# Optimization experiments

Hardware: AMD Instinct MI355X
Metric: run time of the kernel (lower is better)

Reference implementation:

```python
import jax, jax.numpy as jnp
import numpy as np

EPS = 1e-12  # tf.nn.l2_normalize epsilon
ALPHA = 0.9  # hard-negative threshold factor (function default)


def l2_normalize(x):
    # matches tf.nn.l2_normalize: x / sqrt(max(sum(x^2), eps))
    return x * jax.lax.rsqrt(jnp.maximum(jnp.sum(x * x, axis=-1, keepdims=True), EPS))


def setup_inputs() -> dict:
    key = jax.random.key(0)
    k1, k2, k3, k4, k5 = jax.random.split(key, 5)
    B, N, K, D, C = 16, 8, 2048, 512, 11
    return {
        "predicted_vectors": jax.random.normal(k1, (B, C, D), dtype=jnp.float32),
        "positive_vectors": jax.random.normal(k2, (B, N, D), dtype=jnp.float32),
        "negative_gallery": jax.random.normal(k3, (B, N, K, D), dtype=jnp.float32),
        "cluster_centers": jax.random.normal(k4, (C, D), dtype=jnp.float32),
        "positive_categories": jax.random.randint(k5, (B, N), 0, 12, dtype=jnp.int32),
    }


def reference(predicted_vectors, positive_vectors, negative_gallery, cluster_centers, positive_categories):
    # center-base combined contrastive loss (IQON3000, categories 1-11)
    cat_idx = jnp.clip(positive_categories - 1, 0, 10)                 # (B, N)
    # gather predicted slot per category: (B, N, D)
    pred_sel = jnp.take_along_axis(predicted_vectors, cat_idx[..., None], axis=1)
    centers = cluster_centers[cat_idx]                                  # (B, N, D)
    pred_norm = l2_normalize(pred_sel - centers)                        # (B, N, D)
    pos_norm = l2_normalize(positive_vectors - centers)                 # (B, N, D)
    neg_norm = l2_normalize(negative_gallery - centers[:, :, None, :])  # (B, N, K, D)

    sim_pos = jnp.sum(pred_norm * pos_norm, axis=-1)                    # (B, N)
    sim_neg = jnp.einsum('bnd,bnkd->bnk', pred_norm, neg_norm)          # (B, N, K)

    thresh = ALPHA * sim_pos[..., None]
    hard_mask = (sim_neg - sim_pos[..., None] >= thresh).astype(jnp.float32)

    exp_pos = jnp.exp(sim_pos)                                          # sims bounded in [-1,1]
    neg_sum = jnp.sum(jnp.exp(sim_neg) * hard_mask, axis=-1)
    denom = jnp.maximum(exp_pos + neg_sum, 1e-7)
    loss = -jnp.log(exp_pos / denom)
    return jnp.mean(loss)
```

## Files before the change

kernel.cpp:

```cpp
#include <hip/hip_runtime.h>
#include <math.h>

#define BB 16
#define NN 8
#define KK 2048
#define DD 512
#define CC 11
#define BN (BB*NN)
#define NCHUNK 16
#define KCHUNK (KK/NCHUNK)
#define EPSN 1e-12f
#define ALPHA 0.9f

struct f8 { float v[8]; };

__device__ __forceinline__ f8 load8(const float* base, int l) {
    const float4* p = (const float4*)base;
    float4 x = p[l];
    float4 y = p[l + 64];
    f8 r;
    r.v[0] = x.x; r.v[1] = x.y; r.v[2] = x.z; r.v[3] = x.w;
    r.v[4] = y.x; r.v[5] = y.y; r.v[6] = y.z; r.v[7] = y.w;
    return r;
}

__device__ __forceinline__ float wave_reduce(float v) {
    #pragma unroll
    for (int off = 1; off < 64; off <<= 1)
        v += __shfl_xor(v, off, 64);
    return v;
}

__device__ __forceinline__ int clamp_cat(int c) {
    c = c - 1;
    return c < 0 ? 0 : (c > 10 ? 10 : c);
}

__global__ __launch_bounds__(64)
void k1_simpos(const float* __restrict__ pred, const float* __restrict__ pos,
               const float* __restrict__ centers, const int* __restrict__ cats,
               float* __restrict__ simpos) {
    int bn = blockIdx.x;
    int b  = bn / NN;
    int l  = threadIdx.x;
    int cat = clamp_cat(cats[bn]);

    f8 pr = load8(pred + ((size_t)b * CC + cat) * DD, l);
    f8 cc = load8(centers + (size_t)cat * DD, l);
    f8 po = load8(pos + (size_t)bn * DD, l);

    float ssa = 0.f, ssb = 0.f;
    float a[8], p[8];
    #pragma unroll
    for (int j = 0; j < 8; ++j) {
        a[j] = pr.v[j] - cc.v[j];
        p[j] = po.v[j] - cc.v[j];
        ssa += a[j] * a[j];
        ssb += p[j] * p[j];
    }
    ssa = wave_reduce(ssa);
    ssb = wave_reduce(ssb);
    float ia = 1.0f / sqrtf(fmaxf(ssa, EPSN));
    float ib = 1.0f / sqrtf(fmaxf(ssb, EPSN));

    float dp = 0.f;
    #pragma unroll
    for (int j = 0; j < 8; ++j)
        dp += (a[j] * ia) * (p[j] * ib);
    dp = wave_reduce(dp);

    if (l == 0) simpos[bn] = dp;
}

__global__ __launch_bounds__(256)
void k2_neg(const float* __restrict__ pred, const float* __restrict__ neg,
            const float* __restrict__ centers, const int* __restrict__ cats,
            const float* __restrict__ simpos, float* __restrict__ partials) {
    int blk   = blockIdx.x;
    int bn    = blk / NCHUNK;
    int chunk = blk % NCHUNK;
    int b     = bn / NN;
    int wave  = threadIdx.x >> 6;
    int l     = threadIdx.x & 63;

    int cat = clamp_cat(cats[bn]);

    f8 cc = load8(centers + (size_t)cat * DD, l);
    f8 pr = load8(pred + ((size_t)b * CC + cat) * DD, l);

    float pn[8];
    float ss = 0.f;
    #pragma unroll
    for (int j = 0; j < 8; ++j) {
        pn[j] = pr.v[j] - cc.v[j];
        ss += pn[j] * pn[j];
    }
    ss = wave_reduce(ss);
    float inv = 1.0f / sqrtf(fmaxf(ss, EPSN));
    #pragma unroll
    for (int j = 0; j < 8; ++j) pn[j] *= inv;

    float sp = simpos[bn];
    float acc = 0.f;

    const float* nbase = neg + ((size_t)bn * KK + (size_t)chunk * KCHUNK) * DD;

    for (int i = wave; i < KCHUNK; i += 4) {
        f8 nv = load8(nbase + (size_t)i * DD, l);
        float ds = 0.f, s2 = 0.f;
        #pragma unroll
        for (int j = 0; j < 8; ++j) {
            float d = nv.v[j] - cc.v[j];
            ds += pn[j] * d;
            s2 += d * d;
        }
        #pragma unroll
        for (int off = 1; off < 64; off <<= 1) {
            ds += __shfl_xor(ds, off, 64);
            s2 += __shfl_xor(s2, off, 64);
        }
        float sn = ds * (1.0f / sqrtf(fmaxf(s2, EPSN)));
        if (sn - sp >= ALPHA * sp) acc += expf(sn);
    }

    __shared__ float sacc[4];
    if (l == 0) sacc[wave] = acc;
    __syncthreads();
    if (threadIdx.x == 0)
        partials[blk] = sacc[0] + sacc[1] + sacc[2] + sacc[3];
}

__global__ __launch_bounds__(128)
void k3_final(const float* __restrict__ simpos, const float* __restrict__ partials,
              float* __restrict__ out) {
    int bn = threadIdx.x;
    float ns = 0.f;
    for (int i = 0; i < NCHUNK; ++i)
        ns += partials[bn * NCHUNK + i];
    float sp = simpos[bn];
    float ep = expf(sp);
    float denom = fmaxf(ep + ns, 1e-7f);
    float loss = -logf(ep / denom);

    __shared__ float s[BN];
    s[bn] = loss;
    __syncthreads();
    #pragma unroll
    for (int st = 64; st > 0; st >>= 1) {
        if (bn < st) s[bn] += s[bn + st];
        __syncthreads();
    }
    if (bn == 0) out[0] = s[0] / (float)BN;
}

extern "C" void kernel_launch(void* const* d_in, const int* in_sizes, int n_in,
                              void* d_out, int out_size, void* d_ws, size_t ws_size,
                              hipStream_t stream) {
    const float* pred    = (const float*)d_in[0];
    const float* pos     = (const float*)d_in[1];
    const float* neg     = (const float*)d_in[2];
    const float* centers = (const float*)d_in[3];
    const int*   cats    = (const int*)d_in[4];

    float* out = (float*)d_out;

    float* simpos   = (float*)d_ws;
    float* partials = simpos + BN;

    k1_simpos<<<BN, 64, 0, stream>>>(pred, pos, centers, cats, simpos);
    k2_neg<<<BN * NCHUNK, 256, 0, stream>>>(pred, neg, centers, cats, simpos, partials);
    k3_final<<<1, 128, 0, stream>>>(simpos, partials, out);
}
```

Baseline: 105.1 us.

## Process two negatives per wave with half-wave reductions and register prefetch

In the negative-similarity kernel, each wave now splits into two 32-lane halves. Each half handles one negative vector of 16 floats per lane, so the cross-lane reduction needs 5 shuffle steps instead of 6 and each shuffle serves two vectors. The next negative vector is loaded into registers before the current one is computed, giving software double-buffering. This costs more registers (centers, normalized pred and two float4x4 buffers), which may lower occupancy. The kernel is memory-bound on streaming the 1 GB-scale gallery.

```diff
diff --git a/kernel.cpp b/kernel.cpp
--- a/kernel.cpp
+++ b/kernel.cpp
@@ -24,7 +24,7 @@
     return r;
 }
 
-__device__ __forceinline__ float wave_reduce(float v) {
+__device__ __forceinline__ float wave_reduce64(float v) {
     #pragma unroll
     for (int off = 1; off < 64; off <<= 1)
         v += __shfl_xor(v, off, 64);
@@ -58,8 +58,8 @@
         ssa += a[j] * a[j];
         ssb += p[j] * p[j];
     }
-    ssa = wave_reduce(ssa);
-    ssb = wave_reduce(ssb);
+    ssa = wave_reduce64(ssa);
+    ssb = wave_reduce64(ssb);
     float ia = 1.0f / sqrtf(fmaxf(ssa, EPSN));
     float ib = 1.0f / sqrtf(fmaxf(ssb, EPSN));
 
@@ -67,7 +67,7 @@
     #pragma unroll
     for (int j = 0; j < 8; ++j)
         dp += (a[j] * ia) * (p[j] * ib);
-    dp = wave_reduce(dp);
+    dp = wave_reduce64(dp);
 
     if (l == 0) simpos[bn] = dp;
 }
@@ -82,46 +82,74 @@
     int b     = bn / NN;
     int wave  = threadIdx.x >> 6;
     int l     = threadIdx.x & 63;
+    int g     = l >> 5;
+    int sub   = l & 31;
 
     int cat = clamp_cat(cats[bn]);
 
-    f8 cc = load8(centers + (size_t)cat * DD, l);
-    f8 pr = load8(pred + ((size_t)b * CC + cat) * DD, l);
-
-    float pn[8];
+    const float4* c4 = (const float4*)(centers + (size_t)cat * DD);
+    const float4* p4 = (const float4*)(pred + ((size_t)b * CC + cat) * DD);
+
+    float cc[16], pn[16];
     float ss = 0.f;
     #pragma unroll
-    for (int j = 0; j < 8; ++j) {
-        pn[j] = pr.v[j] - cc.v[j];
-        ss += pn[j] * pn[j];
-    }
-    ss = wave_reduce(ss);
+    for (int j = 0; j < 4; ++j) {
+        float4 cv = c4[sub + j * 32];
+        float4 pv = p4[sub + j * 32];
+        cc[j*4+0] = cv.x; cc[j*4+1] = cv.y; cc[j*4+2] = cv.z; cc[j*4+3] = cv.w;
+        float d0 = pv.x - cv.x, d1 = pv.y - cv.y, d2 = pv.z - cv.z, d3 = pv.w - cv.w;
+        pn[j*4+0] = d0; pn[j*4+1] = d1; pn[j*4+2] = d2; pn[j*4+3] = d3;
+        ss += d0*d0 + d1*d1 + d2*d2 + d3*d3;
+    }
+    #pragma unroll
+    for (int off = 1; off < 32; off <<= 1) ss += __shfl_xor(ss, off, 64);
     float inv = 1.0f / sqrtf(fmaxf(ss, EPSN));
     #pragma unroll
-    for (int j = 0; j < 8; ++j) pn[j] *= inv;
+    for (int j = 0; j < 16; ++j) pn[j] *= inv;
 
     float sp = simpos[bn];
     float acc = 0.f;
 
-    const float* nbase = neg + ((size_t)bn * KK + (size_t)chunk * KCHUNK) * DD;
-
-    for (int i = wave; i < KCHUNK; i += 4) {
-        f8 nv = load8(nbase + (size_t)i * DD, l);
+    const float4* nb4 = (const float4*)(neg + ((size_t)bn * KK + (size_t)chunk * KCHUNK) * DD);
+    const int V4 = DD / 4;
+
+    float4 cur[4];
+    {
+        const float4* vb = nb4 + (size_t)(2 * wave + g) * V4;
+        #pragma unroll
+        for (int j = 0; j < 4; ++j) cur[j] = vb[sub + j * 32];
+    }
+
+    for (int it = 0; it < 16; ++it) {
+        float4 nxt[4] = {cur[0], cur[1], cur[2], cur[3]};
+        if (it + 1 < 16) {
+            const float4* vb = nb4 + (size_t)(2 * (wave + 4 * (it + 1)) + g) * V4;
+            #pragma unroll
+            for (int j = 0; j < 4; ++j) nxt[j] = vb[sub + j * 32];
+        }
+
         float ds = 0.f, s2 = 0.f;
         #pragma unroll
-        for (int j = 0; j < 8; ++j) {
-            float d = nv.v[j] - cc.v[j];
-            ds += pn[j] * d;
-            s2 += d * d;
+        for (int j = 0; j < 4; ++j) {
+            float d;
+            d = cur[j].x - cc[j*4+0]; ds += pn[j*4+0] * d; s2 += d * d;
+            d = cur[j].y - cc[j*4+1]; ds += pn[j*4+1] * d; s2 += d * d;
+            d = cur[j].z - cc[j*4+2]; ds += pn[j*4+2] * d; s2 += d * d;
+            d = cur[j].w - cc[j*4+3]; ds += pn[j*4+3] * d; s2 += d * d;
         }
         #pragma unroll
-        for (int off = 1; off < 64; off <<= 1) {
+        for (int off = 1; off < 32; off <<= 1) {
             ds += __shfl_xor(ds, off, 64);
             s2 += __shfl_xor(s2, off, 64);
         }
         float sn = ds * (1.0f / sqrtf(fmaxf(s2, EPSN)));
-        if (sn - sp >= ALPHA * sp) acc += expf(sn);
-    }
+        if (sub == 0 && (sn - sp >= ALPHA * sp)) acc += expf(sn);
+
+        #pragma unroll
+        for (int j = 0; j < 4; ++j) cur[j] = nxt[j];
+    }
+
+    acc += __shfl_xor(acc, 32, 64);
 
     __shared__ float sacc[4];
     if (l == 0) sacc[wave] = acc;
```

Result: faster. 101.7 us (-3.3%).
